# Kernel optimization log

Measured on AMD Instinct MI355X. Metric: run time of the kernel, lower is better.

The kernel has to match this reference:

```python
import jax, jax.numpy as jnp
import numpy as np

B, T, E, H, V = 32, 128, 512, 1024, 32000


def setup_inputs() -> dict:
    key = jax.random.key(0)
    ks = jax.random.split(key, 14)
    s = 0.02  # param init scale to keep gates in a sane range
    return {
        "features": jax.random.normal(ks[0], (B, E), jnp.float32),
        "captions": jax.random.randint(ks[1], (B, T), 0, V, jnp.int64),
        "embed_table": jax.random.normal(ks[2], (V, E), jnp.float32) * s,
        "pos_enc": jax.random.normal(ks[3], (1, T, E), jnp.float32) * s,
        "W_ih0": jax.random.normal(ks[4], (4 * H, E), jnp.float32) * s,
        "W_hh0": jax.random.normal(ks[5], (4 * H, H), jnp.float32) * s,
        "b_ih0": jax.random.normal(ks[6], (4 * H,), jnp.float32) * s,
        "b_hh0": jax.random.normal(ks[7], (4 * H,), jnp.float32) * s,
        "W_ih1": jax.random.normal(ks[8], (4 * H, H), jnp.float32) * s,
        "W_hh1": jax.random.normal(ks[9], (4 * H, H), jnp.float32) * s,
        "b_ih1": jax.random.normal(ks[10], (4 * H,), jnp.float32) * s,
        "b_hh1": jax.random.normal(ks[11], (4 * H,), jnp.float32) * s,
        "W_out": jax.random.normal(ks[12], (V, H), jnp.float32) * s,
        "b_out": jax.random.normal(ks[13], (V,), jnp.float32) * s,
    }


def _lstm_cell(h, c, x, W_ih, W_hh, b_ih, b_hh):
    # PyTorch gate order: i, f, g, o
    g = x @ W_ih.T + b_ih + h @ W_hh.T + b_hh  # (B, 4H)
    i, f, gg, o = jnp.split(g, 4, axis=-1)
    c_new = jax.nn.sigmoid(f) * c + jax.nn.sigmoid(i) * jnp.tanh(gg)
    h_new = jax.nn.sigmoid(o) * jnp.tanh(c_new)
    return h_new, c_new


def reference(features, captions, embed_table, pos_enc,
              W_ih0, W_hh0, b_ih0, b_hh0,
              W_ih1, W_hh1, b_ih1, b_hh1,
              W_out, b_out):
    # Teacher forcing ratio = 1.0 (the default): the input at step t is
    # captions[:, t-1], so the whole sequence of inputs is known upfront.
    bsz, seqlen = captions.shape
    hdim = W_hh0.shape[1]
    vocab = W_out.shape[0]
    dt = embed_table.dtype

    # Embedding lookup for all steps; only pos_enc[:, :1, :] is ever added.
    x = embed_table[captions[:, : seqlen - 1]] + pos_enc[0, 0]  # (B, T-1, E)
    x = jnp.swapaxes(x, 0, 1)  # (T-1, B, E) time-major for scan

    h0 = jnp.zeros((bsz, hdim), dt)
    c0 = jnp.zeros((bsz, hdim), dt)
    h1 = jnp.zeros((bsz, hdim), dt)
    c1 = jnp.zeros((bsz, hdim), dt)

    def step(carry, x_t):
        h0, c0, h1, c1 = carry
        h0, c0 = _lstm_cell(h0, c0, x_t, W_ih0, W_hh0, b_ih0, b_hh0)
        h1, c1 = _lstm_cell(h1, c1, h0, W_ih1, W_hh1, b_ih1, b_hh1)
        return (h0, c0, h1, c1), h1

    _, hs = jax.lax.scan(step, (h0, c0, h1, c1), x)  # (T-1, B, H)

    # One big GEMM for the decode projection of all steps.
    logits = jnp.einsum('tbh,vh->btv', hs, W_out) + b_out  # (B, T-1, V)
    outputs = jnp.concatenate(
        [jnp.zeros((bsz, 1, vocab), dt), logits], axis=1)  # outputs[:,0,:]=0
    return outputs
```

## Files before the change

### kernel.cpp

```cpp
#include <hip/hip_runtime.h>
#include <hip/hip_bf16.h>
#include <math.h>

typedef __attribute__((ext_vector_type(4))) float f32x4;
typedef __attribute__((ext_vector_type(8))) short s16x8;
typedef __attribute__((ext_vector_type(4))) unsigned short u16x4;

#define MFMA16(a, b, c) __builtin_amdgcn_mfma_f32_16x16x32_bf16(a, b, c, 0, 0, 0)

static constexpr int BB = 32, TT = 128, EE = 512, HH = 1024, VV = 32000;
static constexpr int FH = 4 * HH;
static constexpr int MROWS = (TT - 1) * BB;
static constexpr int MPAD = 4096;
static constexpr int BH = BB * HH;
static constexpr int NBLK = 256;

__device__ __forceinline__ unsigned short f2bf(float f) {
  unsigned int u = __float_as_uint(f);
  u = (u + 0x7FFFu + ((u >> 16) & 1u)) >> 16;
  return (unsigned short)u;
}
__device__ __forceinline__ float sigf(float x) { return 1.f / (1.f + __expf(-x)); }

__device__ __forceinline__ s16x8 pack8f(const float* p) {
  float4 x = *(const float4*)p;
  float4 y = *(const float4*)(p + 4);
  s16x8 r;
  r[0] = (short)f2bf(x.x); r[1] = (short)f2bf(x.y);
  r[2] = (short)f2bf(x.z); r[3] = (short)f2bf(x.w);
  r[4] = (short)f2bf(y.x); r[5] = (short)f2bf(y.y);
  r[6] = (short)f2bf(y.z); r[7] = (short)f2bf(y.w);
  return r;
}

__device__ __forceinline__ void gl_lds16(const void* g, void* l) {
  __builtin_amdgcn_global_load_lds(
      (const __attribute__((address_space(1))) unsigned int*)g,
      (__attribute__((address_space(3))) unsigned int*)l, 16, 0, 0);
}

__device__ __forceinline__ unsigned ldflag(const unsigned int* p) {
  return __hip_atomic_load(p, __ATOMIC_RELAXED, __HIP_MEMORY_SCOPE_AGENT);
}


__global__ void zero2_k(uint4* __restrict__ p0, int n0, uint4* __restrict__ p1, int n1) {
  int i = blockIdx.x * blockDim.x + threadIdx.x;
  int stride = gridDim.x * blockDim.x;
  uint4 z = {0u, 0u, 0u, 0u};
  for (int k = i; k < n0; k += stride) p0[k] = z;
  for (int k = i; k < n1; k += stride) p1[k] = z;
}

__global__ void cvt2_k(const float4* __restrict__ a, u16x4* __restrict__ ao, int na4,
                       const float4* __restrict__ b, u16x4* __restrict__ bo, int nb4) {
  int i = blockIdx.x * blockDim.x + threadIdx.x;
  int stride = gridDim.x * blockDim.x;
  for (int k = i; k < na4; k += stride) {
    float4 v = a[k];
    u16x4 o;
    o[0] = f2bf(v.x); o[1] = f2bf(v.y); o[2] = f2bf(v.z); o[3] = f2bf(v.w);
    ao[k] = o;
  }
  for (int k = i; k < nb4; k += stride) {
    float4 v = b[k];
    u16x4 o;
    o[0] = f2bf(v.x); o[1] = f2bf(v.y); o[2] = f2bf(v.z); o[3] = f2bf(v.w);
    bo[k] = o;
  }
}

__global__ __launch_bounds__(256) void embed_k(const int* __restrict__ captions,
                                               const float* __restrict__ etab,
                                               const float* __restrict__ pos,
                                               unsigned short* __restrict__ X) {
  const int m = blockIdx.x;
  const int t = m >> 5, b = m & 31;
  if (t < TT - 1) {
    const int tok = captions[b * TT + t];
    const float* er = etab + (size_t)tok * EE;
    for (int e = threadIdx.x; e < EE; e += 256)
      X[(size_t)m * EE + e] = f2bf(er[e] + pos[e]);
  } else {
    for (int e = threadIdx.x; e < EE; e += 256) X[(size_t)m * EE + e] = 0;
  }
}

__global__ void zero_out_t0(float* __restrict__ out) {
  out[(size_t)blockIdx.y * TT * VV + blockIdx.x * 256 + threadIdx.x] = 0.f;
}


__global__ __launch_bounds__(256) void gemm_bt(const unsigned short* __restrict__ A,
                                               const unsigned short* __restrict__ Bm,
                                               int K, int N,
                                               const float* __restrict__ bias0,
                                               const float* __restrict__ bias1,
                                               float* __restrict__ Cout) {
  __shared__ unsigned short As[128 * 64];
  __shared__ unsigned short Bs[128 * 64];
  const int tid = threadIdx.x;
  const int lane = tid & 63, wave = tid >> 6;
  const int wm = wave & 1, wn = wave >> 1;
  const int m0 = blockIdx.x * 128, n0 = blockIdx.y * 128;
  const int sch = (((lane & 7) ^ ((lane >> 3) & 7)) * 8);
  const int srbase = wave * 32 + (lane >> 3);
  f32x4 acc[4][4] = {};

  for (int k0 = 0; k0 < K; k0 += 64) {
    __syncthreads();
#pragma unroll
    for (int i = 0; i < 4; ++i) {
      const int r = srbase + i * 8;
      gl_lds16(&A[(size_t)(m0 + r) * K + k0 + sch], &As[(wave * 4 + i) * 512]);
      gl_lds16(&Bm[(size_t)(n0 + r) * K + k0 + sch], &Bs[(wave * 4 + i) * 512]);
    }
    __syncthreads();
#pragma unroll
    for (int kk = 0; kk < 64; kk += 32) {
      s16x8 af[4], bf[4];
#pragma unroll
      for (int f = 0; f < 4; ++f) {
        const int Ra = wm * 64 + f * 16 + (lane & 15);
        const int Rb = wn * 64 + f * 16 + (lane & 15);
        const int slot = (kk >> 3) + (lane >> 4);
        af[f] = *(const s16x8*)(&As[Ra * 64 + ((slot ^ (Ra & 7)) * 8)]);
        bf[f] = *(const s16x8*)(&Bs[Rb * 64 + ((slot ^ (Rb & 7)) * 8)]);
      }
#pragma unroll
      for (int mi = 0; mi < 4; ++mi)
#pragma unroll
        for (int ni = 0; ni < 4; ++ni)
          acc[mi][ni] = MFMA16(af[mi], bf[ni], acc[mi][ni]);
    }
  }

#pragma unroll
  for (int mi = 0; mi < 4; ++mi) {
#pragma unroll
    for (int ni = 0; ni < 4; ++ni) {
      const int col = n0 + wn * 64 + ni * 16 + (lane & 15);
      float bs = bias0[col] + bias1[col];
      const int mbase = m0 + wm * 64 + mi * 16 + (lane >> 4) * 4;
#pragma unroll
      for (int r = 0; r < 4; ++r) {
        int m = mbase + r;
        if (m < MROWS) Cout[(size_t)m * N + col] = acc[mi][ni][r] + bs;
      }
    }
  }
}


__global__ __launch_bounds__(512, 1) void proj_gemm(const unsigned short* __restrict__ hsA,
                                                    const unsigned short* __restrict__ Woutb,
                                                    const float* __restrict__ bout,
                                                    float* __restrict__ out) {
  __shared__ unsigned short As[2][256 * 64];
  __shared__ unsigned short Bs[2][256 * 64];
  const int tid = threadIdx.x;
  const int lane = tid & 63, wave = tid >> 6;
  const int wm = wave & 1, wn = wave >> 1;
  const int T = blockIdx.x;
  const int bq = T & 15;
  const int j = 2 * (bq & 7) + (bq >> 3);
  const int n = T >> 4;
  const int m0 = j * 256, n0 = n * 256;
  const int sch = (((lane & 7) ^ ((lane >> 3) & 7)) * 8);
  const int rbase = tid >> 3;
  f32x4 acc[8][4] = {};

  auto stageP = [&](int ks, int buf) {
    const int k0 = ks * 64;
#pragma unroll
    for (int i = 0; i < 4; ++i) {
      const int r = rbase + i * 64;
      gl_lds16(&hsA[(size_t)(m0 + r) * HH + k0 + sch], &As[buf][(wave * 64 + i * 512) * 8]);
      gl_lds16(&Woutb[(size_t)(n0 + r) * HH + k0 + sch], &Bs[buf][(wave * 64 + i * 512) * 8]);
    }
  };

  stageP(0, 0);

  for (int ks = 0; ks < 16; ++ks) {
    const int cur = ks & 1;
    if (ks < 15) {
      stageP(ks + 1, cur ^ 1);
      asm volatile("s_waitcnt vmcnt(8)" ::: "memory");
    } else {
      asm volatile("s_waitcnt vmcnt(0)" ::: "memory");
    }
    __builtin_amdgcn_s_barrier();
#pragma unroll
    for (int kk = 0; kk < 64; kk += 32) {
      s16x8 af[8], bf[4];
#pragma unroll
      for (int f = 0; f < 8; ++f) {
        const int Ra = wm * 128 + f * 16 + (lane & 15);
        const int slot = (kk >> 3) + (lane >> 4);
        af[f] = *(const s16x8*)(&As[cur][Ra * 64 + ((slot ^ (Ra & 7)) * 8)]);
      }
#pragma unroll
      for (int f = 0; f < 4; ++f) {
        const int Rb = wn * 64 + f * 16 + (lane & 15);
        const int slot = (kk >> 3) + (lane >> 4);
        bf[f] = *(const s16x8*)(&Bs[cur][Rb * 64 + ((slot ^ (Rb & 7)) * 8)]);
      }
#pragma unroll
      for (int mi = 0; mi < 8; ++mi)
#pragma unroll
        for (int ni = 0; ni < 4; ++ni)
          acc[mi][ni] = MFMA16(af[mi], bf[ni], acc[mi][ni]);
    }
    asm volatile("" ::: "memory");
    __builtin_amdgcn_s_barrier();
  }

#pragma unroll
  for (int mi = 0; mi < 8; ++mi) {
#pragma unroll
    for (int ni = 0; ni < 4; ++ni) {
      const int col = n0 + wn * 64 + ni * 16 + (lane & 15);
      const float bs = bout[col];
      const int mbase = m0 + wm * 128 + mi * 16 + (lane >> 4) * 4;
#pragma unroll
      for (int r2 = 0; r2 < 4; ++r2) {
        const int m = mbase + r2;
        if (m < MROWS) {
          const int tt = m >> 5, b2 = m & 31;
          out[((size_t)b2 * TT + tt + 1) * VV + col] = acc[mi][ni][r2] + bs;
        }
      }
    }
  }
}


__global__ __launch_bounds__(256, 1) void lstm_persist(
    const float* __restrict__ Whh0f, const float* __restrict__ Wih1f,
    const float* __restrict__ Whh1f, const float* __restrict__ G0pre,
    const float* __restrict__ bih1, const float* __restrict__ bhh1,
    unsigned short* __restrict__ h0seq, unsigned short* __restrict__ hseq1,
    unsigned short* __restrict__ hs_all,
    unsigned int* __restrict__ flags0, unsigned int* __restrict__ flags1) {
  __shared__ float parts[4][2][2][16][16];
  const int bid = blockIdx.x;
  const int layer = bid >> 7;
  const int blk = bid & 127;
  const int tid = threadIdx.x, lane = tid & 63, wave = tid >> 6;
  const int jb = blk * 8;
  const int colIdx = lane & 15;
  const int kq = lane >> 4;
  const int wrow0 = (colIdx >> 3) * HH + jb + (colIdx & 7);

  const int cb = tid >> 3, cjj = tid & 7;
  float creg = 0.f;
  float bsum[4];
  if (layer == 1) {
#pragma unroll
    for (int gi = 0; gi < 4; ++gi)
      bsum[gi] = bih1[gi * HH + jb + cjj] + bhh1[gi * HH + jb + cjj];
  }

  s16x8 wreg[16][2];
  const int kb = (layer == 0) ? wave * 256 : (wave & 1) * 512;
  if (layer == 0) {
#pragma unroll
    for (int fi = 0; fi < 2; ++fi) {
      const float* wp = Whh0f + (size_t)(wrow0 + fi * 2 * HH) * HH + kb + kq * 8;
#pragma unroll
      for (int ks = 0; ks < 8; ++ks) wreg[ks][fi] = pack8f(wp + ks * 32);
    }
  } else {
    const float* Wsrc = (wave < 2) ? Wih1f : Whh1f;
#pragma unroll
    for (int fi = 0; fi < 2; ++fi) {
      const float* wp = Wsrc + (size_t)(wrow0 + fi * 2 * HH) * HH + kb + kq * 8;
#pragma unroll
      for (int ks = 0; ks < 16; ++ks) wreg[ks][fi] = pack8f(wp + ks * 32);
    }
  }

  const int frag_off = (kb >> 3) * 256 + kq * 256 + (lane & 15) * 8;

  if (layer == 0) {
    for (int t = 0; t < TT - 1; ++t) {
      float gpre[4];
#pragma unroll
      for (int gi = 0; gi < 4; ++gi)
        gpre[gi] = G0pre[((size_t)t * BB + cb) * FH + gi * HH + jb + cjj];

      if (t > 0 && wave == 0) {
        const unsigned tgt = (unsigned)t;
        for (;;) {
          unsigned a = ldflag(&flags0[(lane * 2 + 0) * 32]);
          unsigned b = ldflag(&flags0[(lane * 2 + 1) * 32]);
          if (__all(min(a, b) >= tgt)) break;
          __builtin_amdgcn_s_sleep(1);
        }
      }
      __syncthreads();
      asm volatile("" ::: "memory");

      const unsigned short* a0 = h0seq + (size_t)t * BH + frag_off;
      const unsigned short* a1 = a0 + 128;
      f32x4 acc00 = {}, acc01 = {}, acc10 = {}, acc11 = {};
#pragma unroll
      for (int ks = 0; ks < 8; ++ks) {
        s16x8 av0 = *(const s16x8*)(a0 + ks * 1024);
        s16x8 av1 = *(const s16x8*)(a1 + ks * 1024);
        acc00 = MFMA16(av0, wreg[ks][0], acc00);
        acc01 = MFMA16(av0, wreg[ks][1], acc01);
        acc10 = MFMA16(av1, wreg[ks][0], acc10);
        acc11 = MFMA16(av1, wreg[ks][1], acc11);
      }
#pragma unroll
      for (int r = 0; r < 4; ++r) {
        parts[wave][0][0][kq * 4 + r][colIdx] = acc00[r];
        parts[wave][0][1][kq * 4 + r][colIdx] = acc01[r];
        parts[wave][1][0][kq * 4 + r][colIdx] = acc10[r];
        parts[wave][1][1][kq * 4 + r][colIdx] = acc11[r];
      }
      __syncthreads();
      float g[4];
#pragma unroll
      for (int gi = 0; gi < 4; ++gi) {
        float s = gpre[gi];
        const int fi = gi >> 1, c = (gi & 1) * 8 + cjj;
#pragma unroll
        for (int w4 = 0; w4 < 4; ++w4) s += parts[w4][cb >> 4][fi][cb & 15][c];
        g[gi] = s;
      }
      const float i_ = sigf(g[0]), f_ = sigf(g[1]), gg = tanhf(g[2]), o_ = sigf(g[3]);
      creg = f_ * creg + i_ * gg;
      *(volatile unsigned short*)&h0seq[(size_t)(t + 1) * BH + blk * 256 + tid] =
          f2bf(o_ * tanhf(creg));

      asm volatile("s_waitcnt vmcnt(0)" ::: "memory");
      __syncthreads();
      if (tid == 0) *(volatile unsigned int*)&flags0[blk * 32] = (unsigned)(t + 1);
    }
  } else {
    for (int t = 1; t < TT; ++t) {
      if (wave == 0) {
        const unsigned t0 = (unsigned)t, t1 = (unsigned)(t - 1);
        for (;;) {
          unsigned a0 = ldflag(&flags0[(lane * 2 + 0) * 32]);
          unsigned b0 = ldflag(&flags0[(lane * 2 + 1) * 32]);
          unsigned a1 = ldflag(&flags1[(lane * 2 + 0) * 32]);
          unsigned b1 = ldflag(&flags1[(lane * 2 + 1) * 32]);
          bool ok = (min(a0, b0) >= t0) && (min(a1, b1) >= t1);
          if (__all(ok)) break;
          __builtin_amdgcn_s_sleep(1);
        }
      }
      __syncthreads();
      asm volatile("" ::: "memory");

      const unsigned short* base = (wave < 2)
                                       ? (h0seq + (size_t)t * BH)
                                       : (hseq1 + (size_t)(t - 1) * BH);
      const unsigned short* a0 = base + frag_off;
      const unsigned short* a1 = a0 + 128;
      f32x4 acc00 = {}, acc01 = {}, acc10 = {}, acc11 = {};
#pragma unroll
      for (int ks = 0; ks < 16; ++ks) {
        s16x8 av0 = *(const s16x8*)(a0 + ks * 1024);
        s16x8 av1 = *(const s16x8*)(a1 + ks * 1024);
        acc00 = MFMA16(av0, wreg[ks][0], acc00);
        acc01 = MFMA16(av0, wreg[ks][1], acc01);
        acc10 = MFMA16(av1, wreg[ks][0], acc10);
        acc11 = MFMA16(av1, wreg[ks][1], acc11);
      }
#pragma unroll
      for (int r = 0; r < 4; ++r) {
        parts[wave][0][0][kq * 4 + r][colIdx] = acc00[r];
        parts[wave][0][1][kq * 4 + r][colIdx] = acc01[r];
        parts[wave][1][0][kq * 4 + r][colIdx] = acc10[r];
        parts[wave][1][1][kq * 4 + r][colIdx] = acc11[r];
      }
      __syncthreads();
      float g[4];
#pragma unroll
      for (int gi = 0; gi < 4; ++gi) {
        float s = bsum[gi];
        const int fi = gi >> 1, c = (gi & 1) * 8 + cjj;
#pragma unroll
        for (int w4 = 0; w4 < 4; ++w4) s += parts[w4][cb >> 4][fi][cb & 15][c];
        g[gi] = s;
      }
      const float i_ = sigf(g[0]), f_ = sigf(g[1]), gg = tanhf(g[2]), o_ = sigf(g[3]);
      creg = f_ * creg + i_ * gg;
      const unsigned short hv = f2bf(o_ * tanhf(creg));
      *(volatile unsigned short*)&hseq1[(size_t)t * BH + blk * 256 + tid] = hv;
      hs_all[(size_t)t * BH + (size_t)cb * HH + jb + cjj] = hv;

      asm volatile("s_waitcnt vmcnt(0)" ::: "memory");
      __syncthreads();
      if (tid == 0) *(volatile unsigned int*)&flags1[blk * 32] = (unsigned)t;
    }
  }
}


extern "C" void kernel_launch(void* const* d_in, const int* in_sizes, int n_in,
                              void* d_out, int out_size, void* d_ws, size_t ws_size,
                              hipStream_t stream) {
  const int* captions = (const int*)d_in[1];
  const float* etab = (const float*)d_in[2];
  const float* pos = (const float*)d_in[3];
  const float* Wih0 = (const float*)d_in[4];
  const float* Whh0 = (const float*)d_in[5];
  const float* bih0 = (const float*)d_in[6];
  const float* bhh0 = (const float*)d_in[7];
  const float* Wih1 = (const float*)d_in[8];
  const float* Whh1 = (const float*)d_in[9];
  const float* bih1 = (const float*)d_in[10];
  const float* bhh1 = (const float*)d_in[11];
  const float* Wout = (const float*)d_in[12];
  const float* bout = (const float*)d_in[13];
  float* out = (float*)d_out;

  char* w = (char*)d_ws;
  auto alloc = [&](size_t bytes) {
    char* p = w;
    w += (bytes + 255) & ~(size_t)255;
    return p;
  };
  unsigned int* flags0 = (unsigned int*)alloc(128 * 128);
  unsigned int* flags1 = (unsigned int*)alloc(128 * 128);
  unsigned short* h0seq = (unsigned short*)alloc((size_t)TT * BH * 2);
  unsigned short* hseq1 = (unsigned short*)alloc((size_t)TT * BH * 2);
  unsigned short* hs_all = (unsigned short*)alloc((size_t)4160 * HH * 2);

  unsigned short* Xb = (unsigned short*)alloc((size_t)MPAD * EE * 2);
  unsigned short* Wih0b = (unsigned short*)alloc((size_t)FH * EE * 2);
  unsigned short* Woutb = (unsigned short*)alloc((size_t)VV * HH * 2);
  float* G0pre = (float*)alloc((size_t)MROWS * FH * 4);

  hipLaunchKernelGGL(zero2_k, dim3(40), dim3(256), 0, stream,
                     (uint4*)flags0, (int)((128 * 128 * 2 + BH * 2) / 16),
                     (uint4*)hseq1, (int)((BH * 2) / 16));
  hipLaunchKernelGGL(cvt2_k, dim3(4096), dim3(256), 0, stream,
                     (const float4*)Wih0, (u16x4*)Wih0b, FH * EE / 4,
                     (const float4*)Wout, (u16x4*)Woutb, VV * HH / 4);
  hipLaunchKernelGGL(embed_k, dim3(MPAD), dim3(256), 0, stream, captions, etab, pos, Xb);
  hipLaunchKernelGGL(gemm_bt, dim3(32, 32), dim3(256), 0, stream, Xb, Wih0b, EE, FH, bih0,
                     bhh0, G0pre);
  hipLaunchKernelGGL(lstm_persist, dim3(NBLK), dim3(256), 0, stream, Whh0, Wih1, Whh1, G0pre,
                     bih1, bhh1, h0seq, hseq1, hs_all, flags0, flags1);
  hipLaunchKernelGGL(proj_gemm, dim3(2000), dim3(512), 0, stream, hs_all + (size_t)BH,
                     Woutb, bout, out);
  hipLaunchKernelGGL(zero_out_t0, dim3(125, 32), dim3(256), 0, stream, out);
}
```

Baseline: 1.265 ms.

## Fuse layer-0 input projection into persistent LSTM and drop separate GEMM

Removes the standalone Wih0 conversion and input-projection GEMM (G0pre), and instead has layer-0 blocks of the persistent LSTM hold Wih0 slices in registers and compute x_t·Wih0 with MFMA each step from a fragment-laid-out bf16 embedding buffer. It also folds the t=0 output zeroing into the projection GEMM and raises wave priority around its MFMA loop. The aim is to cut the fp32 G0pre write and read traffic and several kernel launches, at the cost of more work on the serial recurrence critical path and higher register pressure in layer-0 blocks.

Measured after the change: 1.244 ms. About the same (-1.7%).

```diff
diff --git a/kernel.cpp b/kernel.cpp
--- a/kernel.cpp
+++ b/kernel.cpp
@@ -11,8 +11,8 @@
 static constexpr int BB = 32, TT = 128, EE = 512, HH = 1024, VV = 32000;
 static constexpr int FH = 4 * HH;
 static constexpr int MROWS = (TT - 1) * BB;
-static constexpr int MPAD = 4096;
 static constexpr int BH = BB * HH;
+static constexpr int BE = BB * EE;
 static constexpr int NBLK = 256;
 
 __device__ __forceinline__ unsigned short f2bf(float f) {
@@ -43,6 +43,8 @@
   return __hip_atomic_load(p, __ATOMIC_RELAXED, __HIP_MEMORY_SCOPE_AGENT);
 }
 
+#define FSTRIDE 32
+
 
 __global__ void zero2_k(uint4* __restrict__ p0, int n0, uint4* __restrict__ p1, int n1) {
   int i = blockIdx.x * blockDim.x + threadIdx.x;
@@ -52,8 +54,7 @@
   for (int k = i; k < n1; k += stride) p1[k] = z;
 }
 
-__global__ void cvt2_k(const float4* __restrict__ a, u16x4* __restrict__ ao, int na4,
-                       const float4* __restrict__ b, u16x4* __restrict__ bo, int nb4) {
+__global__ void cvt1_k(const float4* __restrict__ a, u16x4* __restrict__ ao, int na4) {
   int i = blockIdx.x * blockDim.x + threadIdx.x;
   int stride = gridDim.x * blockDim.x;
   for (int k = i; k < na4; k += stride) {
@@ -62,93 +63,19 @@
     o[0] = f2bf(v.x); o[1] = f2bf(v.y); o[2] = f2bf(v.z); o[3] = f2bf(v.w);
     ao[k] = o;
   }
-  for (int k = i; k < nb4; k += stride) {
-    float4 v = b[k];
-    u16x4 o;
-    o[0] = f2bf(v.x); o[1] = f2bf(v.y); o[2] = f2bf(v.z); o[3] = f2bf(v.w);
-    bo[k] = o;
-  }
 }
 
 __global__ __launch_bounds__(256) void embed_k(const int* __restrict__ captions,
                                                const float* __restrict__ etab,
                                                const float* __restrict__ pos,
-                                               unsigned short* __restrict__ X) {
+                                               unsigned short* __restrict__ Xseq) {
   const int m = blockIdx.x;
   const int t = m >> 5, b = m & 31;
-  if (t < TT - 1) {
-    const int tok = captions[b * TT + t];
-    const float* er = etab + (size_t)tok * EE;
-    for (int e = threadIdx.x; e < EE; e += 256)
-      X[(size_t)m * EE + e] = f2bf(er[e] + pos[e]);
-  } else {
-    for (int e = threadIdx.x; e < EE; e += 256) X[(size_t)m * EE + e] = 0;
-  }
-}
-
-__global__ void zero_out_t0(float* __restrict__ out) {
-  out[(size_t)blockIdx.y * TT * VV + blockIdx.x * 256 + threadIdx.x] = 0.f;
-}
-
-
-__global__ __launch_bounds__(256) void gemm_bt(const unsigned short* __restrict__ A,
-                                               const unsigned short* __restrict__ Bm,
-                                               int K, int N,
-                                               const float* __restrict__ bias0,
-                                               const float* __restrict__ bias1,
-                                               float* __restrict__ Cout) {
-  __shared__ unsigned short As[128 * 64];
-  __shared__ unsigned short Bs[128 * 64];
-  const int tid = threadIdx.x;
-  const int lane = tid & 63, wave = tid >> 6;
-  const int wm = wave & 1, wn = wave >> 1;
-  const int m0 = blockIdx.x * 128, n0 = blockIdx.y * 128;
-  const int sch = (((lane & 7) ^ ((lane >> 3) & 7)) * 8);
-  const int srbase = wave * 32 + (lane >> 3);
-  f32x4 acc[4][4] = {};
-
-  for (int k0 = 0; k0 < K; k0 += 64) {
-    __syncthreads();
-#pragma unroll
-    for (int i = 0; i < 4; ++i) {
-      const int r = srbase + i * 8;
-      gl_lds16(&A[(size_t)(m0 + r) * K + k0 + sch], &As[(wave * 4 + i) * 512]);
-      gl_lds16(&Bm[(size_t)(n0 + r) * K + k0 + sch], &Bs[(wave * 4 + i) * 512]);
-    }
-    __syncthreads();
-#pragma unroll
-    for (int kk = 0; kk < 64; kk += 32) {
-      s16x8 af[4], bf[4];
-#pragma unroll
-      for (int f = 0; f < 4; ++f) {
-        const int Ra = wm * 64 + f * 16 + (lane & 15);
-        const int Rb = wn * 64 + f * 16 + (lane & 15);
-        const int slot = (kk >> 3) + (lane >> 4);
-        af[f] = *(const s16x8*)(&As[Ra * 64 + ((slot ^ (Ra & 7)) * 8)]);
-        bf[f] = *(const s16x8*)(&Bs[Rb * 64 + ((slot ^ (Rb & 7)) * 8)]);
-      }
-#pragma unroll
-      for (int mi = 0; mi < 4; ++mi)
-#pragma unroll
-        for (int ni = 0; ni < 4; ++ni)
-          acc[mi][ni] = MFMA16(af[mi], bf[ni], acc[mi][ni]);
-    }
-  }
-
-#pragma unroll
-  for (int mi = 0; mi < 4; ++mi) {
-#pragma unroll
-    for (int ni = 0; ni < 4; ++ni) {
-      const int col = n0 + wn * 64 + ni * 16 + (lane & 15);
-      float bs = bias0[col] + bias1[col];
-      const int mbase = m0 + wm * 64 + mi * 16 + (lane >> 4) * 4;
-#pragma unroll
-      for (int r = 0; r < 4; ++r) {
-        int m = mbase + r;
-        if (m < MROWS) Cout[(size_t)m * N + col] = acc[mi][ni][r] + bs;
-      }
-    }
-  }
+  const int tok = captions[b * TT + t];
+  const float* er = etab + (size_t)tok * EE;
+  unsigned short* xt = Xseq + (size_t)t * BE;
+  for (int e = threadIdx.x; e < EE; e += 256)
+    xt[(e >> 3) * 256 + b * 8 + (e & 7)] = f2bf(er[e] + pos[e]);
 }
 
 
@@ -191,6 +118,7 @@
       asm volatile("s_waitcnt vmcnt(0)" ::: "memory");
     }
     __builtin_amdgcn_s_barrier();
+    __builtin_amdgcn_s_setprio(1);
 #pragma unroll
     for (int kk = 0; kk < 64; kk += 32) {
       s16x8 af[8], bf[4];
@@ -212,6 +140,7 @@
         for (int ni = 0; ni < 4; ++ni)
           acc[mi][ni] = MFMA16(af[mi], bf[ni], acc[mi][ni]);
     }
+    __builtin_amdgcn_s_setprio(0);
     asm volatile("" ::: "memory");
     __builtin_amdgcn_s_barrier();
   }
@@ -233,13 +162,22 @@
       }
     }
   }
+
+  if (j == 0) {
+    for (int i = tid; i < 32 * 256; i += 512) {
+      const int b2 = i >> 8, c = i & 255;
+      out[(size_t)b2 * TT * VV + n0 + c] = 0.f;
+    }
+  }
 }
 
 
 __global__ __launch_bounds__(256, 1) void lstm_persist(
-    const float* __restrict__ Whh0f, const float* __restrict__ Wih1f,
-    const float* __restrict__ Whh1f, const float* __restrict__ G0pre,
+    const float* __restrict__ Whh0f, const float* __restrict__ Wih0f,
+    const float* __restrict__ Wih1f, const float* __restrict__ Whh1f,
+    const float* __restrict__ bih0, const float* __restrict__ bhh0,
     const float* __restrict__ bih1, const float* __restrict__ bhh1,
+    const unsigned short* __restrict__ Xseq,
     unsigned short* __restrict__ h0seq, unsigned short* __restrict__ hseq1,
     unsigned short* __restrict__ hs_all,
     unsigned int* __restrict__ flags0, unsigned int* __restrict__ flags1) {
@@ -256,20 +194,29 @@
   const int cb = tid >> 3, cjj = tid & 7;
   float creg = 0.f;
   float bsum[4];
-  if (layer == 1) {
+  if (layer == 0) {
+#pragma unroll
+    for (int gi = 0; gi < 4; ++gi)
+      bsum[gi] = bih0[gi * HH + jb + cjj] + bhh0[gi * HH + jb + cjj];
+  } else {
 #pragma unroll
     for (int gi = 0; gi < 4; ++gi)
       bsum[gi] = bih1[gi * HH + jb + cjj] + bhh1[gi * HH + jb + cjj];
   }
 
   s16x8 wreg[16][2];
+  s16x8 wregx[4][2];
   const int kb = (layer == 0) ? wave * 256 : (wave & 1) * 512;
+  const int kbx = wave * 128;
   if (layer == 0) {
 #pragma unroll
     for (int fi = 0; fi < 2; ++fi) {
       const float* wp = Whh0f + (size_t)(wrow0 + fi * 2 * HH) * HH + kb + kq * 8;
 #pragma unroll
       for (int ks = 0; ks < 8; ++ks) wreg[ks][fi] = pack8f(wp + ks * 32);
+      const float* wpx = Wih0f + (size_t)(wrow0 + fi * 2 * HH) * EE + kbx + kq * 8;
+#pragma unroll
+      for (int ks = 0; ks < 4; ++ks) wregx[ks][fi] = pack8f(wpx + ks * 32);
     }
   } else {
     const float* Wsrc = (wave < 2) ? Wih1f : Whh1f;
@@ -282,19 +229,15 @@
   }
 
   const int frag_off = (kb >> 3) * 256 + kq * 256 + (lane & 15) * 8;
+  const int frag_offX = (wave * 16 + kq) * 256 + (lane & 15) * 8;
 
   if (layer == 0) {
     for (int t = 0; t < TT - 1; ++t) {
-      float gpre[4];
-#pragma unroll
-      for (int gi = 0; gi < 4; ++gi)
-        gpre[gi] = G0pre[((size_t)t * BB + cb) * FH + gi * HH + jb + cjj];
-
       if (t > 0 && wave == 0) {
         const unsigned tgt = (unsigned)t;
         for (;;) {
-          unsigned a = ldflag(&flags0[(lane * 2 + 0) * 32]);
-          unsigned b = ldflag(&flags0[(lane * 2 + 1) * 32]);
+          unsigned a = ldflag(&flags0[(lane * 2 + 0) * FSTRIDE]);
+          unsigned b = ldflag(&flags0[(lane * 2 + 1) * FSTRIDE]);
           if (__all(min(a, b) >= tgt)) break;
           __builtin_amdgcn_s_sleep(1);
         }
@@ -302,9 +245,20 @@
       __syncthreads();
       asm volatile("" ::: "memory");
 
+      const unsigned short* x0 = Xseq + (size_t)t * BE + frag_offX;
+      const unsigned short* x1 = x0 + 128;
       const unsigned short* a0 = h0seq + (size_t)t * BH + frag_off;
       const unsigned short* a1 = a0 + 128;
       f32x4 acc00 = {}, acc01 = {}, acc10 = {}, acc11 = {};
+#pragma unroll
+      for (int ks = 0; ks < 4; ++ks) {
+        s16x8 xv0 = *(const s16x8*)(x0 + ks * 1024);
+        s16x8 xv1 = *(const s16x8*)(x1 + ks * 1024);
+        acc00 = MFMA16(xv0, wregx[ks][0], acc00);
+        acc01 = MFMA16(xv0, wregx[ks][1], acc01);
+        acc10 = MFMA16(xv1, wregx[ks][0], acc10);
+        acc11 = MFMA16(xv1, wregx[ks][1], acc11);
+      }
 #pragma unroll
       for (int ks = 0; ks < 8; ++ks) {
         s16x8 av0 = *(const s16x8*)(a0 + ks * 1024);
@@ -325,7 +279,7 @@
       float g[4];
 #pragma unroll
       for (int gi = 0; gi < 4; ++gi) {
-        float s = gpre[gi];
+        float s = bsum[gi];
         const int fi = gi >> 1, c = (gi & 1) * 8 + cjj;
 #pragma unroll
         for (int w4 = 0; w4 < 4; ++w4) s += parts[w4][cb >> 4][fi][cb & 15][c];
@@ -338,18 +292,18 @@
 
       asm volatile("s_waitcnt vmcnt(0)" ::: "memory");
       __syncthreads();
-      if (tid == 0) *(volatile unsigned int*)&flags0[blk * 32] = (unsigned)(t + 1);
+      if (tid == 0) *(volatile unsigned int*)&flags0[blk * FSTRIDE] = (unsigned)(t + 1);
     }
   } else {
     for (int t = 1; t < TT; ++t) {
       if (wave == 0) {
         const unsigned t0 = (unsigned)t, t1 = (unsigned)(t - 1);
         for (;;) {
-          unsigned a0 = ldflag(&flags0[(lane * 2 + 0) * 32]);
-          unsigned b0 = ldflag(&flags0[(lane * 2 + 1) * 32]);
-          unsigned a1 = ldflag(&flags1[(lane * 2 + 0) * 32]);
-          unsigned b1 = ldflag(&flags1[(lane * 2 + 1) * 32]);
-          bool ok = (min(a0, b0) >= t0) && (min(a1, b1) >= t1);
+          unsigned a0f = ldflag(&flags0[(lane * 2 + 0) * FSTRIDE]);
+          unsigned b0f = ldflag(&flags0[(lane * 2 + 1) * FSTRIDE]);
+          unsigned a1f = ldflag(&flags1[(lane * 2 + 0) * FSTRIDE]);
+          unsigned b1f = ldflag(&flags1[(lane * 2 + 1) * FSTRIDE]);
+          bool ok = (min(a0f, b0f) >= t0) && (min(a1f, b1f) >= t1);
           if (__all(ok)) break;
           __builtin_amdgcn_s_sleep(1);
         }
@@ -397,7 +351,7 @@
 
       asm volatile("s_waitcnt vmcnt(0)" ::: "memory");
       __syncthreads();
-      if (tid == 0) *(volatile unsigned int*)&flags1[blk * 32] = (unsigned)t;
+      if (tid == 0) *(volatile unsigned int*)&flags1[blk * FSTRIDE] = (unsigned)t;
     }
   }
 }
@@ -432,24 +386,17 @@
   unsigned short* h0seq = (unsigned short*)alloc((size_t)TT * BH * 2);
   unsigned short* hseq1 = (unsigned short*)alloc((size_t)TT * BH * 2);
   unsigned short* hs_all = (unsigned short*)alloc((size_t)4160 * HH * 2);
-
-  unsigned short* Xb = (unsigned short*)alloc((size_t)MPAD * EE * 2);
-  unsigned short* Wih0b = (unsigned short*)alloc((size_t)FH * EE * 2);
+  unsigned short* Xseq = (unsigned short*)alloc((size_t)TT * BE * 2);
   unsigned short* Woutb = (unsigned short*)alloc((size_t)VV * HH * 2);
-  float* G0pre = (float*)alloc((size_t)MROWS * FH * 4);
 
   hipLaunchKernelGGL(zero2_k, dim3(40), dim3(256), 0, stream,
                      (uint4*)flags0, (int)((128 * 128 * 2 + BH * 2) / 16),
                      (uint4*)hseq1, (int)((BH * 2) / 16));
-  hipLaunchKernelGGL(cvt2_k, dim3(4096), dim3(256), 0, stream,
-                     (const float4*)Wih0, (u16x4*)Wih0b, FH * EE / 4,
-                     (const float4*)Wout, (u16x4*)Woutb, VV * HH / 4);
-  hipLaunchKernelGGL(embed_k, dim3(MPAD), dim3(256), 0, stream, captions, etab, pos, Xb);
-  hipLaunchKernelGGL(gemm_bt, dim3(32, 32), dim3(256), 0, stream, Xb, Wih0b, EE, FH, bih0,
-                     bhh0, G0pre);
-  hipLaunchKernelGGL(lstm_persist, dim3(NBLK), dim3(256), 0, stream, Whh0, Wih1, Whh1, G0pre,
-                     bih1, bhh1, h0seq, hseq1, hs_all, flags0, flags1);
+  hipLaunchKernelGGL(cvt1_k, dim3(4096), dim3(256), 0, stream, (const float4*)Wout,
+                     (u16x4*)Woutb, VV * HH / 4);
+  hipLaunchKernelGGL(embed_k, dim3(MROWS), dim3(256), 0, stream, captions, etab, pos, Xseq);
+  hipLaunchKernelGGL(lstm_persist, dim3(NBLK), dim3(256), 0, stream, Whh0, Wih0, Wih1, Whh1,
+                     bih0, bhh0, bih1, bhh1, Xseq, h0seq, hseq1, hs_all, flags0, flags1);
   hipLaunchKernelGGL(proj_gemm, dim3(2000), dim3(512), 0, stream, hs_all + (size_t)BH,
                      Woutb, bout, out);
-  hipLaunchKernelGGL(zero_out_t0, dim3(125, 32), dim3(256), 0, stream, out);
-}
+}
```
